# Optimization experiments

Hardware: AMD Instinct MI355X
Metric: run time of the kernel (lower is better)

Reference implementation:

```python
import jax, jax.numpy as jnp
import numpy as np

N = 50000      # num nodes
E = 800000     # edges per hypergraph (avg degree 16)
G = 3          # hyper_edge_num
D_IN = 128
D_OUT = 128


def setup_inputs() -> dict:
    key = jax.random.key(0)
    ks = jax.random.split(key, 6)
    company_emb = jax.random.normal(ks[0], (N, D_IN), dtype=jnp.float32)
    # nn.Linear weight [out, in], glorot-ish scaling
    W = jax.random.normal(ks[1], (D_OUT, D_IN), dtype=jnp.float32) / np.sqrt(D_IN).astype(np.float32)
    alpha = jax.random.normal(ks[2], (G, 1), dtype=jnp.float32)
    edge_rows = jax.random.randint(ks[3], (G, E), 0, N, dtype=jnp.int32)
    edge_cols = jax.random.randint(ks[4], (G, E), 0, N, dtype=jnp.int32)
    edge_vals = jax.random.normal(ks[5], (G, E), dtype=jnp.float32)
    return {
        "company_emb": company_emb,
        "W": W,
        "alpha": alpha,
        "edge_rows": edge_rows,
        "edge_cols": edge_cols,
        "edge_vals": edge_vals,
    }


def reference(company_emb, W, alpha, edge_rows, edge_cols, edge_vals):
    # shared dense projection: h = X @ W^T, [N, D_OUT]
    h = company_emb @ W.T

    def spmm(rows, cols, vals):
        # sparse Laplacian (COO) @ h : gather source rows, scale, scatter-add to dest rows
        msg = vals[:, None] * h[cols]                     # [E, D_OUT]
        return jax.ops.segment_sum(msg, rows, num_segments=N)

    aggs = jax.vmap(spmm)(edge_rows, edge_cols, edge_vals)  # [G, N, D_OUT]
    gate = jax.nn.sigmoid(alpha[:, 0])                       # [G]
    # res = sum_g sigmoid(alpha_g) * (L_g @ h)
    return jnp.einsum('g,gnd->nd', gate, aggs)
```

## Files before the change

### kernel.cpp

```cpp
#include <hip/hip_runtime.h>
#include <math.h>

#define NNODES 50000
#define NEDGE  800000
#define NG     3
#define D      128
#define GE     (NG*NEDGE)
#define NBUK   782
#define CH     4096
#define NBLK   ((GE + CH - 1) / CH)
#define CAP2   3456

typedef __attribute__((ext_vector_type(8))) short bf16x8;
typedef __attribute__((ext_vector_type(4))) float f32x4;

__device__ __forceinline__ unsigned short f2bf(float f) {
    unsigned u = __float_as_uint(f);
    return (unsigned short)((u + 0x7fffu + ((u >> 16) & 1u)) >> 16);
}

__global__ void k_wprep(const float* __restrict__ W, uint4* __restrict__ Wf) {
    const int t = threadIdx.x;
    for (int i = t; i < 2048; i += 256) {
        const int nt   = i >> 8;
        const int kc   = (i >> 6) & 3;
        const int lane = i & 63;
        const int n  = nt * 16 + (lane & 15);
        const int k0 = kc * 32 + (lane >> 4) * 8;
        const float* src = W + (size_t)n * 128 + k0;
        unsigned u0 = (unsigned)f2bf(src[0]) | ((unsigned)f2bf(src[1]) << 16);
        unsigned u1 = (unsigned)f2bf(src[2]) | ((unsigned)f2bf(src[3]) << 16);
        unsigned u2 = (unsigned)f2bf(src[4]) | ((unsigned)f2bf(src[5]) << 16);
        unsigned u3 = (unsigned)f2bf(src[6]) | ((unsigned)f2bf(src[7]) << 16);
        Wf[i] = make_uint4(u0, u1, u2, u3);
    }
}

__global__ __launch_bounds__(256) void k_gemm(const float* __restrict__ X,
                                              const uint4* __restrict__ Wf,
                                              unsigned short* __restrict__ hb16) {
    __shared__ uint4 Wl[2048];
    const int t = threadIdx.x;
#pragma unroll
    for (int j = 0; j < 8; ++j) Wl[t + j * 256] = Wf[t + j * 256];
    __syncthreads();

    const int w    = t >> 6;
    const int lane = t & 63;
    const int q    = lane >> 4;
    const int ml   = lane & 15;
    const int m0   = blockIdx.x * 64 + w * 16;

    int xr = m0 + ml; if (xr >= NNODES) xr = NNODES - 1;
    const float* xrow = X + (size_t)xr * 128;

    bf16x8 xf[4];
#pragma unroll
    for (int kc = 0; kc < 4; ++kc) {
        const int k0 = kc * 32 + q * 8;
        float4 a = *(const float4*)(xrow + k0);
        float4 b = *(const float4*)(xrow + k0 + 4);
        bf16x8 v;
        v[0] = (short)f2bf(a.x); v[1] = (short)f2bf(a.y);
        v[2] = (short)f2bf(a.z); v[3] = (short)f2bf(a.w);
        v[4] = (short)f2bf(b.x); v[5] = (short)f2bf(b.y);
        v[6] = (short)f2bf(b.z); v[7] = (short)f2bf(b.w);
        xf[kc] = v;
    }

#pragma unroll
    for (int nt = 0; nt < 8; ++nt) {
        f32x4 acc = {0.f, 0.f, 0.f, 0.f};
#pragma unroll
        for (int kc = 0; kc < 4; ++kc) {
            const bf16x8 wf = *(const bf16x8*)&Wl[(nt * 4 + kc) * 64 + lane];
            acc = __builtin_amdgcn_mfma_f32_16x16x32_bf16(xf[kc], wf, acc, 0, 0, 0);
        }
#pragma unroll
        for (int r = 0; r < 4; ++r) {
            const int row = m0 + q * 4 + r;
            if (row < NNODES)
                hb16[(size_t)row * 128 + nt * 16 + ml] = f2bf(acc[r]);
        }
    }
}

__global__ __launch_bounds__(256) void k_bin(const int* __restrict__ rows,
                                             const int* __restrict__ cols,
                                             const float* __restrict__ vals,
                                             const float* __restrict__ alpha,
                                             uint2* __restrict__ out1,
                                             int* __restrict__ off1T) {
    __shared__ uint2 stg[CH];
    __shared__ unsigned short rnk[CH];
    __shared__ int sE[1024];
    __shared__ int wtot[4];
    const int t   = threadIdx.x;
    const int blk = blockIdx.x;
    const int start = blk * CH;
    const int end   = (start + CH < GE) ? (start + CH) : GE;

    const float g0 = 1.0f / (1.0f + __expf(-alpha[0]));
    const float g1 = 1.0f / (1.0f + __expf(-alpha[1]));
    const float g2 = 1.0f / (1.0f + __expf(-alpha[2]));

#pragma unroll
    for (int j = 0; j < 4; ++j) sE[t + j * 256] = 0;
    __syncthreads();

    for (int idx = start + t, k = t; idx < end; idx += 256, k += 256) {
        const int r = rows[idx];
        const int c = cols[idx];
        const float v = vals[idx];
        const float gv = v * (idx < NEDGE ? g0 : (idx < 2 * NEDGE ? g1 : g2));
        uint2 rec;
        rec.x = ((unsigned)r << 16) | (unsigned)c;
        rec.y = __float_as_uint(gv);
        stg[k] = rec;
        rnk[k] = (unsigned short)atomicAdd(&sE[r >> 6], 1);
    }
    __syncthreads();

    const int lane = t & 63;
    const int w    = t >> 6;
    int4 v4 = *(int4*)&sE[4 * t];
    const int l1 = v4.x + v4.y;
    const int l2 = l1 + v4.z;
    const int l3 = l2 + v4.w;
    int s = l3;
#pragma unroll
    for (int off = 1; off < 64; off <<= 1) {
        int n = __shfl_up(s, off);
        if (lane >= off) s += n;
    }
    if (lane == 63) wtot[w] = s;
    const int waveExcl = s - l3;
    __syncthreads();
    int cross = 0;
    for (int j = 0; j < w; ++j) cross += wtot[j];
    const int b0 = cross + waveExcl;
    int4 e4;
    e4.x = b0; e4.y = b0 + v4.x; e4.z = b0 + l1; e4.w = b0 + l2;
    *(int4*)&sE[4 * t] = e4;
    __syncthreads();

    for (int b = t; b < NBUK; b += 256)
        off1T[(size_t)b * NBLK + blk] = sE[b];
    if (t == 0) off1T[(size_t)NBUK * NBLK + blk] = end - start;

    for (int idx = start + t, k = t; idx < end; idx += 256, k += 256) {
        const uint2 rec = stg[k];
        const int b = (int)(rec.x >> 22);
        out1[(size_t)blk * CH + sE[b] + (int)rnk[k]] = rec;
    }
}

__global__ __launch_bounds__(512) void k_agg2(const unsigned* __restrict__ hbits,
                                              const uint2* __restrict__ out1,
                                              const int* __restrict__ off1T,
                                              float* __restrict__ out) {
    __shared__ uint2 stg[CAP2];
    __shared__ int rh[64], rbase[64], rcur[64];
    const int t = threadIdx.x;
    const int b = blockIdx.x;

    if (t < 64) rh[t] = 0;
    __syncthreads();

    int s0 = 0, e0 = 0, s1 = 0, e1 = 0;
    if (t < NBLK) {
        s0 = off1T[(size_t)b * NBLK + t];
        e0 = off1T[(size_t)(b + 1) * NBLK + t];
    }
    if (t + 512 < NBLK) {
        s1 = off1T[(size_t)b * NBLK + t + 512];
        e1 = off1T[(size_t)(b + 1) * NBLK + t + 512];
    }

    {
        const unsigned* seg = (const unsigned*)(out1 + (size_t)t * CH);
        for (int i = s0; i < e0; ++i)
            atomicAdd(&rh[(seg[2 * i] >> 16) & 63u], 1);
        if (t + 512 < NBLK) {
            const unsigned* seg2 = (const unsigned*)(out1 + (size_t)(t + 512) * CH);
            for (int i = s1; i < e1; ++i)
                atomicAdd(&rh[(seg2[2 * i] >> 16) & 63u], 1);
        }
    }
    __syncthreads();

    if (t < 64) {
        const int pad = (rh[t] + 1) & ~1;
        int sv = pad;
#pragma unroll
        for (int off = 1; off < 64; off <<= 1) {
            int n = __shfl_up(sv, off);
            if (t >= off) sv += n;
        }
        int base = sv - pad;
        if (base > CAP2) base = CAP2;
        rbase[t] = base;
        rcur[t]  = base;
    }
    __syncthreads();

    {
        const uint2* seg = out1 + (size_t)t * CH;
        for (int i = s0; i < e0; ++i) {
            const uint2 rec = seg[i];
            const int pos = atomicAdd(&rcur[(rec.x >> 16) & 63u], 1);
            if (pos < CAP2) stg[pos] = rec;
        }
        if (t + 512 < NBLK) {
            const uint2* seg2 = out1 + (size_t)(t + 512) * CH;
            for (int i = s1; i < e1; ++i) {
                const uint2 rec = seg2[i];
                const int pos = atomicAdd(&rcur[(rec.x >> 16) & 63u], 1);
                if (pos < CAP2) stg[pos] = rec;
            }
        }
    }
    __syncthreads();

    const int w    = t >> 6;
    const int lane = t & 63;
    for (int k = 0; k < 8; ++k) {
        const int lr  = (w << 3) + k;
        const int row = (b << 6) + lr;
        const int s   = rbase[lr];
        int cnt = rh[lr];
        if (s + cnt > CAP2) cnt = (CAP2 > s) ? (CAP2 - s) : 0;
        float2 acc = make_float2(0.f, 0.f);
        int i = 0;
        for (; i + 8 <= cnt; i += 8) {
            const uint4 q0 = *(const uint4*)&stg[s + i];
            const uint4 q1 = *(const uint4*)&stg[s + i + 2];
            const uint4 q2 = *(const uint4*)&stg[s + i + 4];
            const uint4 q3 = *(const uint4*)&stg[s + i + 6];
            unsigned cm[8] = {q0.x, q0.z, q1.x, q1.z, q2.x, q2.z, q3.x, q3.z};
            unsigned vv[8] = {q0.y, q0.w, q1.y, q1.w, q2.y, q2.w, q3.y, q3.w};
            unsigned hb[8];
#pragma unroll
            for (int j = 0; j < 8; ++j)
                hb[j] = hbits[(size_t)(cm[j] & 0xffffu) * 64 + lane];
#pragma unroll
            for (int j = 0; j < 8; ++j) {
                const float v = __uint_as_float(vv[j]);
                acc.x += v * __uint_as_float(hb[j] << 16);
                acc.y += v * __uint_as_float(hb[j] & 0xffff0000u);
            }
        }
        for (; i < cnt; ++i) {
            const uint2 m = stg[s + i];
            const unsigned hbv = hbits[(size_t)(m.x & 0xffffu) * 64 + lane];
            const float v = __uint_as_float(m.y);
            acc.x += v * __uint_as_float(hbv << 16);
            acc.y += v * __uint_as_float(hbv & 0xffff0000u);
        }
        if (row < NNODES)
            ((float2*)out)[(size_t)row * 64 + lane] = acc;
    }
}

extern "C" void kernel_launch(void* const* d_in, const int* in_sizes, int n_in,
                              void* d_out, int out_size, void* d_ws, size_t ws_size,
                              hipStream_t stream) {
    const float* X     = (const float*)d_in[0];
    const float* W     = (const float*)d_in[1];
    const float* alpha = (const float*)d_in[2];
    const int*   rows  = (const int*)d_in[3];
    const int*   cols  = (const int*)d_in[4];
    const float* vals  = (const float*)d_in[5];
    float* out = (float*)d_out;

    char* ws = (char*)d_ws;
    unsigned*       hbits = (unsigned*)(ws + 0);
    unsigned short* hb16  = (unsigned short*)(ws + 0);
    uint2*          out1  = (uint2*)(ws + 12800000);
    int*            off1T = (int*)  (ws + 32002048);
    uint4*          Wf    = (uint4*)(ws + 33837408);

    hipLaunchKernelGGL(k_wprep, dim3(1), dim3(256), 0, stream, W, Wf);
    hipLaunchKernelGGL(k_gemm, dim3(NBUK), dim3(256), 0, stream, X, Wf, hb16);
    hipLaunchKernelGGL(k_bin, dim3(NBLK), dim3(256), 0, stream,
                       rows, cols, vals, alpha, out1, off1T);
    hipLaunchKernelGGL(k_agg2, dim3(NBUK), dim3(512), 0, stream,
                       hbits, out1, off1T, out);
}
```

Baseline: 260.4 us.

## Counting-sort agg2 edges by row and column sub-bucket via index permutation

Replaces the two-pass histogram-then-scatter staging in the second aggregation kernel with a single pass. Records are copied contiguously into shared memory at prefix-sum offsets while each one gets a per-key rank. Keys are (row, column high bits), so edges within a row are ordered by source column bucket, which is meant to improve cache locality of the hbits gathers. It also removes the second global read of the bucketed edge records. In exchange it adds a 1024-entry key scan, an order array, and an indirect shared-memory lookup per edge in the inner loop.

```diff
diff --git a/kernel.cpp b/kernel.cpp
--- a/kernel.cpp
+++ b/kernel.cpp
@@ -10,6 +10,7 @@
 #define CH     4096
 #define NBLK   ((GE + CH - 1) / CH)
 #define CAP2   3456
+#define NKEY2  1024
 
 typedef __attribute__((ext_vector_type(8))) short bf16x8;
 typedef __attribute__((ext_vector_type(4))) float f32x4;
@@ -160,98 +161,128 @@
                                               const int* __restrict__ off1T,
                                               float* __restrict__ out) {
     __shared__ uint2 stg[CAP2];
-    __shared__ int rh[64], rbase[64], rcur[64];
+    __shared__ unsigned short order[CAP2];
+    __shared__ unsigned short rnk[CAP2];
+    __shared__ int kbase[NKEY2];
+    __shared__ int rbase[65];
+    __shared__ int wtot[8];
     const int t = threadIdx.x;
     const int b = blockIdx.x;
-
-    if (t < 64) rh[t] = 0;
-    __syncthreads();
-
-    int s0 = 0, e0 = 0, s1 = 0, e1 = 0;
-    if (t < NBLK) {
-        s0 = off1T[(size_t)b * NBLK + t];
-        e0 = off1T[(size_t)(b + 1) * NBLK + t];
-    }
+    const int lane = t & 63;
+    const int w    = t >> 6;
+
+    kbase[2 * t] = 0; kbase[2 * t + 1] = 0;
+
+    const int s0 = off1T[(size_t)b * NBLK + t];
+    const int e0 = off1T[(size_t)(b + 1) * NBLK + t];
+    int s1 = 0, e1 = 0;
+    int myLen = e0 - s0;
     if (t + 512 < NBLK) {
         s1 = off1T[(size_t)b * NBLK + t + 512];
         e1 = off1T[(size_t)(b + 1) * NBLK + t + 512];
-    }
+        myLen += e1 - s1;
+    }
+
+    int s = myLen;
+#pragma unroll
+    for (int off = 1; off < 64; off <<= 1) {
+        int n = __shfl_up(s, off);
+        if (lane >= off) s += n;
+    }
+    if (lane == 63) wtot[w] = s;
+    const int waveExcl = s - myLen;
+    __syncthreads();
+    int cross = 0;
+    for (int j = 0; j < w; ++j) cross += wtot[j];
+    const int base = cross + waveExcl;
 
     {
-        const unsigned* seg = (const unsigned*)(out1 + (size_t)t * CH);
-        for (int i = s0; i < e0; ++i)
-            atomicAdd(&rh[(seg[2 * i] >> 16) & 63u], 1);
+        int p = base;
+        const uint2* seg = out1 + (size_t)t * CH;
+        for (int i = s0; i < e0; ++i, ++p) {
+            if (p < CAP2) {
+                const uint2 rec = seg[i];
+                stg[p] = rec;
+                const int key = (int)((rec.x >> 16) & 63u) * 16 + (int)((rec.x & 0xffffu) >> 12);
+                rnk[p] = (unsigned short)atomicAdd(&kbase[key], 1);
+            }
+        }
         if (t + 512 < NBLK) {
-            const unsigned* seg2 = (const unsigned*)(out1 + (size_t)(t + 512) * CH);
-            for (int i = s1; i < e1; ++i)
-                atomicAdd(&rh[(seg2[2 * i] >> 16) & 63u], 1);
-        }
-    }
-    __syncthreads();
-
-    if (t < 64) {
-        const int pad = (rh[t] + 1) & ~1;
-        int sv = pad;
+            const uint2* seg2 = out1 + (size_t)(t + 512) * CH;
+            for (int i = s1; i < e1; ++i, ++p) {
+                if (p < CAP2) {
+                    const uint2 rec = seg2[i];
+                    stg[p] = rec;
+                    const int key = (int)((rec.x >> 16) & 63u) * 16 + (int)((rec.x & 0xffffu) >> 12);
+                    rnk[p] = (unsigned short)atomicAdd(&kbase[key], 1);
+                }
+            }
+        }
+    }
+    __syncthreads();
+
+    {
+        const int c0 = kbase[2 * t];
+        const int c1 = kbase[2 * t + 1];
+        const int run = c0 + c1;
+        int sv = run;
 #pragma unroll
         for (int off = 1; off < 64; off <<= 1) {
             int n = __shfl_up(sv, off);
-            if (t >= off) sv += n;
-        }
-        int base = sv - pad;
-        if (base > CAP2) base = CAP2;
-        rbase[t] = base;
-        rcur[t]  = base;
-    }
+            if (lane >= off) sv += n;
+        }
+        if (lane == 63) wtot[w] = sv;
+        const int wExcl = sv - run;
+        __syncthreads();
+        int cr = 0;
+        for (int j = 0; j < w; ++j) cr += wtot[j];
+        kbase[2 * t]     = cr + wExcl;
+        kbase[2 * t + 1] = cr + wExcl + c0;
+        if (t == 511) rbase[64] = cr + sv;
+    }
+    __syncthreads();
+    if (t < 64) rbase[t] = kbase[t * 16];
     __syncthreads();
 
     {
-        const uint2* seg = out1 + (size_t)t * CH;
-        for (int i = s0; i < e0; ++i) {
-            const uint2 rec = seg[i];
-            const int pos = atomicAdd(&rcur[(rec.x >> 16) & 63u], 1);
-            if (pos < CAP2) stg[pos] = rec;
-        }
-        if (t + 512 < NBLK) {
-            const uint2* seg2 = out1 + (size_t)(t + 512) * CH;
-            for (int i = s1; i < e1; ++i) {
-                const uint2 rec = seg2[i];
-                const int pos = atomicAdd(&rcur[(rec.x >> 16) & 63u], 1);
-                if (pos < CAP2) stg[pos] = rec;
-            }
-        }
-    }
-    __syncthreads();
-
-    const int w    = t >> 6;
-    const int lane = t & 63;
+        const int lim = (base + myLen < CAP2) ? (base + myLen) : CAP2;
+        for (int p = base; p < lim; ++p) {
+            const unsigned rx = stg[p].x;
+            const int key = (int)((rx >> 16) & 63u) * 16 + (int)((rx & 0xffffu) >> 12);
+            const int pos = kbase[key] + (int)rnk[p];
+            if (pos < CAP2) order[pos] = (unsigned short)p;
+        }
+    }
+    __syncthreads();
+
     for (int k = 0; k < 8; ++k) {
         const int lr  = (w << 3) + k;
         const int row = (b << 6) + lr;
-        const int s   = rbase[lr];
-        int cnt = rh[lr];
-        if (s + cnt > CAP2) cnt = (CAP2 > s) ? (CAP2 - s) : 0;
+        const int sR  = rbase[lr];
+        int cnt = rbase[lr + 1] - sR;
+        if (sR + cnt > CAP2) cnt = (CAP2 > sR) ? (CAP2 - sR) : 0;
         float2 acc = make_float2(0.f, 0.f);
         int i = 0;
         for (; i + 8 <= cnt; i += 8) {
-            const uint4 q0 = *(const uint4*)&stg[s + i];
-            const uint4 q1 = *(const uint4*)&stg[s + i + 2];
-            const uint4 q2 = *(const uint4*)&stg[s + i + 4];
-            const uint4 q3 = *(const uint4*)&stg[s + i + 6];
-            unsigned cm[8] = {q0.x, q0.z, q1.x, q1.z, q2.x, q2.z, q3.x, q3.z};
-            unsigned vv[8] = {q0.y, q0.w, q1.y, q1.w, q2.y, q2.w, q3.y, q3.w};
+            int idx8[8];
+#pragma unroll
+            for (int j = 0; j < 8; ++j) idx8[j] = order[sR + i + j];
+            uint2 m[8];
+#pragma unroll
+            for (int j = 0; j < 8; ++j) m[j] = stg[idx8[j]];
             unsigned hb[8];
 #pragma unroll
             for (int j = 0; j < 8; ++j)
-                hb[j] = hbits[(size_t)(cm[j] & 0xffffu) * 64 + lane];
+                hb[j] = hbits[(size_t)(m[j].x & 0xffffu) * 64 + lane];
 #pragma unroll
             for (int j = 0; j < 8; ++j) {
-                const float v = __uint_as_float(vv[j]);
+                const float v = __uint_as_float(m[j].y);
                 acc.x += v * __uint_as_float(hb[j] << 16);
                 acc.y += v * __uint_as_float(hb[j] & 0xffff0000u);
             }
         }
         for (; i < cnt; ++i) {
-            const uint2 m = stg[s + i];
+            const uint2 m = stg[order[sR + i]];
             const unsigned hbv = hbits[(size_t)(m.x & 0xffffu) * 64 + lane];
             const float v = __uint_as_float(m.y);
             acc.x += v * __uint_as_float(hbv << 16);
```

After: 267.9 us. 1.03x slower.
